# Kernel tuning notes

Measured on AMD Instinct MI355X. Metric: run time of the kernel, lower is better.

The kernel has to match this reference:

```python
import jax, jax.numpy as jnp
import numpy as np

BASE = 10000.0

def rotate_half(x):
    # interleaved pairs: (x0, x1, x2, x3, ...) -> (-x1, x0, -x3, x2, ...)
    x2 = x.reshape(x.shape[:-1] + (-1, 2))
    a, b = x2[..., 0], x2[..., 1]
    return jnp.stack((-b, a), axis=-1).reshape(x.shape)

def rope_tables(seq_len, head_dim, dtype):
    inv_freq = 1.0 / (BASE ** (jnp.arange(0, head_dim, 2, dtype=jnp.float32) / head_dim))
    t = jnp.arange(seq_len, dtype=jnp.float32)
    freqs = jnp.outer(t, inv_freq)                      # [s, head_dim//2]
    cos = jnp.repeat(jnp.cos(freqs), 2, axis=-1)        # '... d -> ... (d 2)'
    sin = jnp.repeat(jnp.sin(freqs), 2, axis=-1)
    # seq_dimension = -3 for [b, s, h, d] tensors -> broadcast over heads
    return cos[:, None, :].astype(dtype), sin[:, None, :].astype(dtype)

def setup_inputs() -> dict:
    key = jax.random.key(0)
    kx, kw1, kw2 = jax.random.split(key, 3)
    b, s, d = 4, 2048, 2048
    h = 16
    x = jax.random.normal(kx, (b, s, d), dtype=jnp.float32)
    # causal mask: True above the diagonal = masked positions
    attn_mask = jnp.triu(jnp.ones((s, s), dtype=bool), k=1)
    Wqkv_w = jax.random.normal(kw1, (d, 3 * d), dtype=jnp.float32) / np.sqrt(d)
    Wqkv_b = jnp.zeros((3 * d,), dtype=jnp.float32)
    Wout_w = jax.random.normal(kw2, (d, d), dtype=jnp.float32) / np.sqrt(d)
    Wout_b = jnp.zeros((d,), dtype=jnp.float32)
    return {"x": x, "attn_mask": attn_mask, "Wqkv_w": Wqkv_w, "Wqkv_b": Wqkv_b,
            "Wout_w": Wout_w, "Wout_b": Wout_b, "num_heads": 16}

def reference(x, attn_mask, Wqkv_w, Wqkv_b, Wout_w, Wout_b, num_heads):
    b, s, d = x.shape
    h = num_heads
    hd = d // h
    qkv = jnp.einsum('bsd,de->bse', x, Wqkv_w) + Wqkv_b        # [b, s, 3d]
    qkv = qkv.reshape(b, s, 3, h, hd)
    q, k, v = qkv[:, :, 0], qkv[:, :, 1], qkv[:, :, 2]          # [b, s, h, hd]
    cos, sin = rope_tables(s, hd, x.dtype)                      # [s, 1, hd]
    q = q * cos + rotate_half(q) * sin
    k = k * cos + rotate_half(k) * sin
    scale = 1.0 / np.sqrt(hd).astype(np.float32)
    scores = jnp.einsum('bqhd,bkhd->bhqk', q, k) * scale        # [b, h, s, s]
    scores = jnp.where(attn_mask, -jnp.inf, scores)
    attn = jax.nn.softmax(scores, axis=-1)
    ctx = jnp.einsum('bhqk,bkhd->bqhd', attn, v)                # [b, s, h, hd]
    ctx = ctx.reshape(b, s, d)
    return jnp.einsum('bsd,de->bse', ctx, Wout_w) + Wout_b
```

## Files before the change

### kernel.cpp

```cpp
#include <hip/hip_runtime.h>

#define BB 4
#define SS 2048
#define DD 2048
#define HH 16
#define HD 128
#define D3 6144

typedef __attribute__((ext_vector_type(8))) short short8;
typedef __attribute__((ext_vector_type(4))) float float4v;

#define MFMA16(a, b, c) __builtin_amdgcn_mfma_f32_16x16x32_bf16(a, b, c, 0, 0, 0)

#define GLL16(g, l)                                                     \
    __builtin_amdgcn_global_load_lds(                                   \
        (__attribute__((address_space(1))) void*)(g),                   \
        (__attribute__((address_space(3))) void*)(l), 16, 0, 0)

__device__ __forceinline__ unsigned short f2b(float f) {
    union { float f; unsigned u; } v;
    v.f = f;
    unsigned r = v.u + 0x7FFFu + ((v.u >> 16) & 1u);
    return (unsigned short)(r >> 16);
}
__device__ __forceinline__ float b2f(unsigned short h) {
    union { unsigned u; float f; } v;
    v.u = ((unsigned)h) << 16;
    return v.f;
}

__global__ void cast_f32_bf16(const float* __restrict__ in,
                              unsigned short* __restrict__ out) {
    int i = (blockIdx.x * 256 + threadIdx.x) * 4;
    float4 v = *(const float4*)(in + i);
    ushort4 o;
    o.x = f2b(v.x); o.y = f2b(v.y); o.z = f2b(v.z); o.w = f2b(v.w);
    *(ushort4*)(out + i) = o;
}

__global__ void transpose_cast(const float* __restrict__ in,
                               unsigned short* __restrict__ out, int R, int C) {
    __shared__ float tile[32][33];
    int c0 = blockIdx.x * 32, r0 = blockIdx.y * 32;
    int tc = threadIdx.x & 31, tr = threadIdx.x >> 5;
#pragma unroll
    for (int i = 0; i < 4; ++i) {
        int r = tr + i * 8;
        tile[r][tc] = in[(size_t)(r0 + r) * C + c0 + tc];
    }
    __syncthreads();
#pragma unroll
    for (int i = 0; i < 4; ++i) {
        int wr = tr + i * 8;
        out[(size_t)(c0 + wr) * R + r0 + tc] = f2b(tile[tc][wr]);
    }
}

__global__ void vtrans(const unsigned short* __restrict__ qkv,
                       unsigned short* __restrict__ vT) {
    __shared__ unsigned short tile[32][33];
    int bh = blockIdx.z, b = bh >> 4, h = bh & 15;
    int s0 = blockIdx.x * 32, d0 = blockIdx.y * 32;
    int tc = threadIdx.x & 31, tr = threadIdx.x >> 5;
    const unsigned short* src = qkv + (size_t)b * SS * D3 + 4096 + h * HD;
#pragma unroll
    for (int i = 0; i < 4; ++i) {
        int sl = tr + i * 8;
        tile[sl][tc] = src[(size_t)(s0 + sl) * D3 + d0 + tc];
    }
    __syncthreads();
    unsigned short* dst = vT + (size_t)bh * HD * SS;
#pragma unroll
    for (int i = 0; i < 4; ++i) {
        int dl = tr + i * 8;
        dst[(size_t)(d0 + dl) * SS + s0 + tc] = tile[tc][dl];
    }
}

template <int BF16OUT>
__global__ __launch_bounds__(512, 2) void gemm256(
    const unsigned short* __restrict__ A,
    const unsigned short* __restrict__ Bt,
    const float* __restrict__ bias,
    void* __restrict__ Cout, int M, int N, int K) {
    __shared__ unsigned short As[2][256 * 64];
    __shared__ unsigned short Bs[2][256 * 64];

    const int nbx = N >> 8;
    const int lin = blockIdx.y * nbx + blockIdx.x;
    const int cpx = (nbx * (M >> 8)) >> 3;
    const int wg = (lin & 7) * cpx + (lin >> 3);
    const int n0 = (wg % nbx) * 256, m0 = (wg / nbx) * 256;

    const int t = threadIdx.x, lane = t & 63, w = t >> 6;
    const int quad = lane >> 4, lr = lane & 15;
    const int wm = (w >> 2) * 128, wn = (w & 3) * 64;

    const int sr = lane >> 3;
    const int ss = (lane & 7) ^ sr;
    const unsigned short* Ag = A + (size_t)(m0 + w * 32 + sr) * K + ss * 8;
    const unsigned short* Bg = Bt + (size_t)(n0 + w * 32 + sr) * K + ss * 8;

    float4v acc[8][4] = {};
    short8 af[4][2], b0[2][2], b1[2][2];

#define STAGE_A(buf, k0)                                                     \
    do {                                                                     \
        _Pragma("unroll") for (int r = 0; r < 4; ++r)                        \
            GLL16(Ag + (k0) + (size_t)r * 8 * K,                             \
                  &As[buf][(w * 32 + r * 8) * 64]);                          \
    } while (0)
#define STAGE_B(buf, k0)                                                     \
    do {                                                                     \
        _Pragma("unroll") for (int r = 0; r < 4; ++r)                        \
            GLL16(Bg + (k0) + (size_t)r * 8 * K,                             \
                  &Bs[buf][(w * 32 + r * 8) * 64]);                          \
    } while (0)
#define LDA(dst, mh)                                                         \
    do {                                                                     \
        _Pragma("unroll") for (int i = 0; i < 4; ++i)                        \
            _Pragma("unroll") for (int kk = 0; kk < 2; ++kk)                 \
                dst[i][kk] = *(const short8*)&As[cur][                       \
                    (wm + (mh)*64 + i * 16 + lr) * 64 +                      \
                    (((kk * 4 + quad) ^ (lr & 7)) * 8)];                     \
    } while (0)
#define LDB(dst, nh)                                                         \
    do {                                                                     \
        _Pragma("unroll") for (int j = 0; j < 2; ++j)                        \
            _Pragma("unroll") for (int kk = 0; kk < 2; ++kk)                 \
                dst[j][kk] = *(const short8*)&Bs[cur][                       \
                    (wn + (nh)*32 + j * 16 + lr) * 64 +                      \
                    (((kk * 4 + quad) ^ (lr & 7)) * 8)];                     \
    } while (0)
#define MM(ar, br, io, jo)                                                   \
    do {                                                                     \
        __builtin_amdgcn_s_setprio(1);                                       \
        _Pragma("unroll") for (int kk = 0; kk < 2; ++kk)                     \
            _Pragma("unroll") for (int i = 0; i < 4; ++i)                    \
                _Pragma("unroll") for (int j = 0; j < 2; ++j)                \
                    acc[(io) + i][(jo) + j] = MFMA16(                        \
                        ar[i][kk], br[j][kk], acc[(io) + i][(jo) + j]);      \
        __builtin_amdgcn_s_setprio(0);                                       \
    } while (0)

    const int NT = K >> 6;
    STAGE_A(0, 0);
    STAGE_B(0, 0);

    for (int tk = 0; tk < NT; ++tk) {
        const int cur = tk & 1, nxt = cur ^ 1;
        const size_t k0n = (size_t)(tk + 1 == NT ? 0 : tk + 1) << 6;

        STAGE_A(nxt, k0n);
        asm volatile("s_waitcnt vmcnt(4)" ::: "memory");
        __builtin_amdgcn_s_barrier();
        __builtin_amdgcn_sched_barrier(0);
        LDA(af, 0);
        LDB(b0, 0);
        __builtin_amdgcn_s_barrier();
        asm volatile("s_waitcnt lgkmcnt(0)" ::: "memory");
        __builtin_amdgcn_sched_barrier(0);
        MM(af, b0, 0, 0);
        __builtin_amdgcn_s_barrier();
        STAGE_B(nxt, k0n);
        LDB(b1, 1);
        __builtin_amdgcn_s_barrier();
        asm volatile("s_waitcnt lgkmcnt(0)" ::: "memory");
        __builtin_amdgcn_sched_barrier(0);
        MM(af, b1, 0, 2);
        __builtin_amdgcn_s_barrier();
        LDA(af, 1);
        __builtin_amdgcn_s_barrier();
        asm volatile("s_waitcnt lgkmcnt(0)" ::: "memory");
        __builtin_amdgcn_sched_barrier(0);
        MM(af, b0, 4, 0);
        __builtin_amdgcn_s_barrier();
        MM(af, b1, 4, 2);
        __builtin_amdgcn_s_barrier();
    }
    asm volatile("s_waitcnt vmcnt(0)" ::: "memory");

#pragma unroll
    for (int jj = 0; jj < 4; ++jj) {
        const int n = n0 + wn + jj * 16 + lr;
        const float bv = bias[n];
#pragma unroll
        for (int ii = 0; ii < 8; ++ii)
#pragma unroll
            for (int r = 0; r < 4; ++r) {
                const int m = m0 + wm + ii * 16 + quad * 4 + r;
                const float v = acc[ii][jj][r] + bv;
                if (BF16OUT)
                    ((unsigned short*)Cout)[(size_t)m * N + n] = f2b(v);
                else
                    ((float*)Cout)[(size_t)m * N + n] = v;
            }
    }
#undef STAGE_A
#undef STAGE_B
#undef LDA
#undef LDB
#undef MM
}

__global__ void rope_kernel(unsigned short* __restrict__ qkv) {
    int tid = blockIdx.x * 256 + threadIdx.x;
    int i4 = tid & 15;
    int h = (tid >> 4) & 15;
    int s = (tid >> 8) & 2047;
    int b = tid >> 19;
    size_t off = ((size_t)(b * SS + s)) * D3 + h * HD + i4 * 8;
    unsigned short* q = qkv + off;
    unsigned short* k = q + 2048;
    short8 qv = *(short8*)q, kv = *(short8*)k;
    const float L2IF = 0.2076205059304601f;
    const float R2PI = 0.15915494309189535f;
    short8 qo, ko;
#pragma unroll
    for (int j = 0; j < 4; ++j) {
        int i = i4 * 4 + j;
        float invr = exp2f(-(float)i * L2IF) * R2PI;
        float rev = (float)s * invr;
        float rr = rev - floorf(rev);
        float sn = __builtin_amdgcn_sinf(rr);
        float cs = __builtin_amdgcn_cosf(rr);
        float a0 = b2f((unsigned short)qv[2 * j]);
        float a1 = b2f((unsigned short)qv[2 * j + 1]);
        qo[2 * j] = (short)f2b(a0 * cs - a1 * sn);
        qo[2 * j + 1] = (short)f2b(a1 * cs + a0 * sn);
        float c0 = b2f((unsigned short)kv[2 * j]);
        float c1 = b2f((unsigned short)kv[2 * j + 1]);
        ko[2 * j] = (short)f2b(c0 * cs - c1 * sn);
        ko[2 * j + 1] = (short)f2b(c1 * cs + c0 * sn);
    }
    *(short8*)q = qo;
    *(short8*)k = ko;
}

__global__ __launch_bounds__(256) void attn_kernel(
    const unsigned short* __restrict__ qkv,
    const unsigned short* __restrict__ vT,
    unsigned short* __restrict__ ctx) {
    __shared__ unsigned short Ks[2][64 * 128];
    __shared__ unsigned short Vs[2][128 * 64];
    __shared__ unsigned short PT[4][32][40];
    const int bh = blockIdx.y, b = bh >> 4, h = bh & 15;
    const int t = threadIdx.x, w = t >> 6, lane = t & 63;
    const int quad = lane >> 4, lr = lane & 15;
    const unsigned short* qbase = qkv + (size_t)b * SS * D3 + h * HD;
    const unsigned short* kbase = qbase + 2048;
    const unsigned short* vtb = vT + (size_t)bh * HD * SS;
    const float SCL2E = 0.12751741769976451f;
    const float NB16 = -23.083120654223414f;
    const int q0a = blockIdx.x * 128;
    const int q0b = (15 - (int)blockIdx.x) * 128;
    const int nta = (q0a >> 6) + 2, ntb = (q0b >> 6) + 2, ntot = nta + ntb;
    const int kr = lane >> 4, kg = lane & 15;
    const int vr = lane >> 3, vg = lane & 7;

    auto stage = [&](int k0, int bi) {
        unsigned short* KD = Ks[bi];
        unsigned short* VD = Vs[bi];
#pragma unroll
        for (int u = 0; u < 4; ++u) {
            int row = w * 16 + u * 4 + kr;
            int g = kg ^ (row & 15);
            GLL16(kbase + (size_t)(k0 + row) * D3 + g * 8,
                  &KD[(w * 16 + u * 4) * 128]);
        }
#pragma unroll
        for (int u = 0; u < 4; ++u) {
            int row = w * 32 + u * 8 + vr;
            int g = vg ^ (row & 7);
            GLL16(vtb + (size_t)row * SS + k0 + g * 8,
                  &VD[(w * 32 + u * 8) * 64]);
        }
    };

    int wq = q0a + w * 32;
    short8 qf[2][4];
#pragma unroll
    for (int m = 0; m < 2; ++m)
#pragma unroll
        for (int c = 0; c < 4; ++c)
            qf[m][c] = *(const short8*)(qbase + (size_t)(wq + m * 16 + lr) * D3 +
                                        c * 32 + quad * 8);

    float4v o[2][8] = {};
    float l_lane[2] = {0.f, 0.f};

    auto epilogue = [&]() {
#pragma unroll
        for (int m = 0; m < 2; ++m) {
            float l = l_lane[m];
            l += __shfl_xor(l, 16);
            l += __shfl_xor(l, 32);
#pragma unroll
            for (int r = 0; r < 4; ++r) {
                float linv = 1.0f / __shfl(l, quad * 4 + r);
#pragma unroll
                for (int dc = 0; dc < 8; ++dc) {
                    float val = o[m][dc][r] * linv;
                    ctx[(size_t)(b * SS + wq + m * 16 + quad * 4 + r) * DD +
                        h * HD + dc * 16 + lr] = f2b(val);
                }
            }
        }
    };

    stage(0, 0);

    for (int it = 0; it < ntot; ++it) {
        __syncthreads();
        int nit = it + 1;
        if (nit < ntot) stage((nit < nta ? nit : nit - nta) * 64, nit & 1);
        int k0 = (it < nta ? it : it - nta) * 64;
        const unsigned short* KB = Ks[it & 1];
        const unsigned short* VB = Vs[it & 1];

        if (k0 <= wq + 31) {
            float4v sc[2][4] = {};
#pragma unroll
            for (int c = 0; c < 4; ++c) {
                short8 kf[4];
#pragma unroll
                for (int ks = 0; ks < 4; ++ks)
                    kf[ks] = *(const short8*)&KB[(ks * 16 + lr) * 128 +
                                                 (((c * 4 + quad) ^ lr) * 8)];
#pragma unroll
                for (int ks = 0; ks < 4; ++ks) {
                    sc[0][ks] = MFMA16(kf[ks], qf[0][c], sc[0][ks]);
                    sc[1][ks] = MFMA16(kf[ks], qf[1][c], sc[1][ks]);
                }
            }
            const bool nm = (k0 + 63 > wq);
#pragma unroll
            for (int kc = 0; kc < 2; ++kc) {
#pragma unroll
                for (int m = 0; m < 2; ++m)
#pragma unroll
                    for (int ks2 = 0; ks2 < 2; ++ks2) {
                        int ks = kc * 2 + ks2;
                        unsigned pk[2];
#pragma unroll
                        for (int rp = 0; rp < 2; ++rp) {
                            unsigned lo = 0, hi = 0;
#pragma unroll
                            for (int rr = 0; rr < 2; ++rr) {
                                int r = rp * 2 + rr;
                                float p = exp2f(fmaf(sc[m][ks][r], SCL2E, NB16));
                                if (nm) {
                                    int key = k0 + ks * 16 + quad * 4 + r;
                                    if (key > wq + m * 16 + lr) p = 0.0f;
                                }
                                l_lane[m] += p;
                                union { float f; unsigned u; } pu;
                                pu.f = p;
                                if (rr == 0) lo = pu.u >> 16;
                                else hi = pu.u >> 16;
                            }
                            pk[rp] = lo | (hi << 16);
                        }
                        uint2 pkk = {pk[0], pk[1]};
                        *(uint2*)&PT[w][m * 16 + lr][ks2 * 16 + quad * 4] = pkk;
                    }
                short8 pf0 = *(const short8*)&PT[w][lr][quad * 8];
                short8 pf1 = *(const short8*)&PT[w][16 + lr][quad * 8];
#pragma unroll
                for (int dc = 0; dc < 8; ++dc) {
                    short8 vf = *(const short8*)&VB[(dc * 16 + lr) * 64 +
                                                    (((kc * 4 + quad) ^ (lr & 7)) * 8)];
                    o[0][dc] = MFMA16(pf0, vf, o[0][dc]);
                    o[1][dc] = MFMA16(pf1, vf, o[1][dc]);
                }
            }
        }

        if (it == nta - 1) {
            epilogue();
#pragma unroll
            for (int m = 0; m < 2; ++m) {
                l_lane[m] = 0.f;
#pragma unroll
                for (int dc = 0; dc < 8; ++dc) o[m][dc] = (float4v){0, 0, 0, 0};
            }
            wq = q0b + w * 32;
#pragma unroll
            for (int m = 0; m < 2; ++m)
#pragma unroll
                for (int c = 0; c < 4; ++c)
                    qf[m][c] = *(const short8*)(qbase +
                                                (size_t)(wq + m * 16 + lr) * D3 +
                                                c * 32 + quad * 8);
        }
    }
    epilogue();
}

extern "C" void kernel_launch(void* const* d_in, const int* in_sizes, int n_in,
                              void* d_out, int out_size, void* d_ws, size_t ws_size,
                              hipStream_t stream) {
    const float* x = (const float*)d_in[0];
    const float* Wqkv_w = (const float*)d_in[2];
    const float* Wqkv_b = (const float*)d_in[3];
    const float* Wout_w = (const float*)d_in[4];
    const float* Wout_b = (const float*)d_in[5];
    float* out = (float*)d_out;

    unsigned short* x_bf = (unsigned short*)d_ws;
    unsigned short* wqkv_t = x_bf + 16777216;
    unsigned short* wout_t = wqkv_t + 12582912;
    unsigned short* qkv = wout_t + 4194304;
    unsigned short* ctx = qkv + 50331648;
    unsigned short* vT = x_bf;

    cast_f32_bf16<<<16384, 256, 0, stream>>>(x, x_bf);
    transpose_cast<<<dim3(192, 64), 256, 0, stream>>>(Wqkv_w, wqkv_t, 2048, 6144);
    transpose_cast<<<dim3(64, 64), 256, 0, stream>>>(Wout_w, wout_t, 2048, 2048);
    gemm256<1><<<dim3(24, 32), 512, 0, stream>>>(x_bf, wqkv_t, Wqkv_b, qkv,
                                                 8192, 6144, 2048);
    rope_kernel<<<8192, 256, 0, stream>>>(qkv);
    vtrans<<<dim3(64, 4, 64), 256, 0, stream>>>(qkv, vT);
    attn_kernel<<<dim3(8, 64), 256, 0, stream>>>(qkv, vT, ctx);
    gemm256<0><<<dim3(8, 32), 512, 0, stream>>>(ctx, wout_t, Wout_b, out,
                                                8192, 2048, 2048);
}
```

Baseline: 786.0 us.

## Restructure GEMM into four-stage K=32 pipeline with prefetch three tiles ahead

The 256x256 GEMM's K tile shrinks from 64 to 32 and the shared-memory ring grows from two buffers to four. Global-to-LDS loads now run three iterations ahead, gated by vmcnt(8). The LDS swizzle is reworked for the narrower 32-element rows, and the XCD-aware block remapping is replaced by a plain blockIdx mapping. This aims to hide global-load latency better at the same LDS footprint, but it doubles the number of loop iterations and barriers and drops the L2-locality block ordering.

```diff
diff --git a/kernel.cpp b/kernel.cpp
--- a/kernel.cpp
+++ b/kernel.cpp
@@ -83,99 +83,90 @@
     const unsigned short* __restrict__ Bt,
     const float* __restrict__ bias,
     void* __restrict__ Cout, int M, int N, int K) {
-    __shared__ unsigned short As[2][256 * 64];
-    __shared__ unsigned short Bs[2][256 * 64];
-
-    const int nbx = N >> 8;
-    const int lin = blockIdx.y * nbx + blockIdx.x;
-    const int cpx = (nbx * (M >> 8)) >> 3;
-    const int wg = (lin & 7) * cpx + (lin >> 3);
-    const int n0 = (wg % nbx) * 256, m0 = (wg / nbx) * 256;
-
+    __shared__ unsigned short As[4][256 * 32];
+    __shared__ unsigned short Bs[4][256 * 32];
+
+    const int n0 = blockIdx.x * 256, m0 = blockIdx.y * 256;
     const int t = threadIdx.x, lane = t & 63, w = t >> 6;
     const int quad = lane >> 4, lr = lane & 15;
     const int wm = (w >> 2) * 128, wn = (w & 3) * 64;
 
-    const int sr = lane >> 3;
-    const int ss = (lane & 7) ^ sr;
-    const unsigned short* Ag = A + (size_t)(m0 + w * 32 + sr) * K + ss * 8;
-    const unsigned short* Bg = Bt + (size_t)(n0 + w * 32 + sr) * K + ss * 8;
+    const int sr = lane >> 2;
+    const int sc = ((lane & 3) ^ ((lane >> 3) & 3)) * 8;
+    const unsigned short* Ag = A + (size_t)(m0 + w * 16 + sr) * K + sc;
+    const unsigned short* Bg = Bt + (size_t)(n0 + w * 16 + sr) * K + sc;
+
+    const int rsw = (quad ^ ((lr >> 1) & 3)) * 8;
 
     float4v acc[8][4] = {};
-    short8 af[4][2], b0[2][2], b1[2][2];
-
-#define STAGE_A(buf, k0)                                                     \
-    do {                                                                     \
-        _Pragma("unroll") for (int r = 0; r < 4; ++r)                        \
-            GLL16(Ag + (k0) + (size_t)r * 8 * K,                             \
-                  &As[buf][(w * 32 + r * 8) * 64]);                          \
-    } while (0)
-#define STAGE_B(buf, k0)                                                     \
-    do {                                                                     \
-        _Pragma("unroll") for (int r = 0; r < 4; ++r)                        \
-            GLL16(Bg + (k0) + (size_t)r * 8 * K,                             \
-                  &Bs[buf][(w * 32 + r * 8) * 64]);                          \
-    } while (0)
+    short8 af0[4], af1[4], b0[2], b1[2];
+
+#define SA(buf, rb, k0) \
+    GLL16(Ag + (size_t)(rb) * K + (k0), &As[buf][((rb) + w * 16) * 32])
+#define SB(buf, rb, k0) \
+    GLL16(Bg + (size_t)(rb) * K + (k0), &Bs[buf][((rb) + w * 16) * 32])
+#define STAGE_A(buf, k0) do { SA(buf, 0, k0); SA(buf, 128, k0); } while (0)
+#define STAGE_B(buf, k0) do { SB(buf, 0, k0); SB(buf, 128, k0); } while (0)
 #define LDA(dst, mh)                                                         \
     do {                                                                     \
         _Pragma("unroll") for (int i = 0; i < 4; ++i)                        \
-            _Pragma("unroll") for (int kk = 0; kk < 2; ++kk)                 \
-                dst[i][kk] = *(const short8*)&As[cur][                       \
-                    (wm + (mh)*64 + i * 16 + lr) * 64 +                      \
-                    (((kk * 4 + quad) ^ (lr & 7)) * 8)];                     \
+            dst[i] = *(const short8*)&As[cur][                               \
+                (wm + (mh)*64 + i * 16 + lr) * 32 + rsw];                    \
     } while (0)
 #define LDB(dst, nh)                                                         \
     do {                                                                     \
         _Pragma("unroll") for (int j = 0; j < 2; ++j)                        \
-            _Pragma("unroll") for (int kk = 0; kk < 2; ++kk)                 \
-                dst[j][kk] = *(const short8*)&Bs[cur][                       \
-                    (wn + (nh)*32 + j * 16 + lr) * 64 +                      \
-                    (((kk * 4 + quad) ^ (lr & 7)) * 8)];                     \
+            dst[j] = *(const short8*)&Bs[cur][                               \
+                (wn + (nh)*32 + j * 16 + lr) * 32 + rsw];                    \
     } while (0)
 #define MM(ar, br, io, jo)                                                   \
     do {                                                                     \
         __builtin_amdgcn_s_setprio(1);                                       \
-        _Pragma("unroll") for (int kk = 0; kk < 2; ++kk)                     \
-            _Pragma("unroll") for (int i = 0; i < 4; ++i)                    \
-                _Pragma("unroll") for (int j = 0; j < 2; ++j)                \
-                    acc[(io) + i][(jo) + j] = MFMA16(                        \
-                        ar[i][kk], br[j][kk], acc[(io) + i][(jo) + j]);      \
+        _Pragma("unroll") for (int i = 0; i < 4; ++i)                        \
+            _Pragma("unroll") for (int j = 0; j < 2; ++j)                    \
+                acc[(io) + i][(jo) + j] = MFMA16(                            \
+                    ar[i], br[j], acc[(io) + i][(jo) + j]);                  \
         __builtin_amdgcn_s_setprio(0);                                       \
     } while (0)
-
-    const int NT = K >> 6;
-    STAGE_A(0, 0);
-    STAGE_B(0, 0);
+#define WAIT_LGKM0()                                                         \
+    do {                                                                     \
+        asm volatile("s_waitcnt lgkmcnt(0)" ::: "memory");                   \
+        __builtin_amdgcn_sched_barrier(0);                                   \
+    } while (0)
+
+    const int NT = K >> 5;
+    STAGE_A(0, 0);  STAGE_B(0, 0);
+    STAGE_A(1, 32); STAGE_B(1, 32);
+    STAGE_A(2, 64); STAGE_B(2, 64);
+    asm volatile("s_waitcnt vmcnt(8)" ::: "memory");
+    __builtin_amdgcn_s_barrier();
 
     for (int tk = 0; tk < NT; ++tk) {
-        const int cur = tk & 1, nxt = cur ^ 1;
-        const size_t k0n = (size_t)(tk + 1 == NT ? 0 : tk + 1) << 6;
-
-        STAGE_A(nxt, k0n);
-        asm volatile("s_waitcnt vmcnt(4)" ::: "memory");
-        __builtin_amdgcn_s_barrier();
-        __builtin_amdgcn_sched_barrier(0);
-        LDA(af, 0);
+        const int cur = tk & 3;
+        const int b3 = (tk + 3) & 3;
+        int t3 = tk + 3; if (t3 >= NT) t3 -= NT;
+        const int k3 = t3 << 5;
+
+        LDA(af0, 0);
         LDB(b0, 0);
-        __builtin_amdgcn_s_barrier();
-        asm volatile("s_waitcnt lgkmcnt(0)" ::: "memory");
-        __builtin_amdgcn_sched_barrier(0);
-        MM(af, b0, 0, 0);
-        __builtin_amdgcn_s_barrier();
-        STAGE_B(nxt, k0n);
+        STAGE_A(b3, k3);
+        __builtin_amdgcn_s_barrier();
+        WAIT_LGKM0();
+        MM(af0, b0, 0, 0);
+        __builtin_amdgcn_s_barrier();
         LDB(b1, 1);
-        __builtin_amdgcn_s_barrier();
-        asm volatile("s_waitcnt lgkmcnt(0)" ::: "memory");
-        __builtin_amdgcn_sched_barrier(0);
-        MM(af, b1, 0, 2);
-        __builtin_amdgcn_s_barrier();
-        LDA(af, 1);
-        __builtin_amdgcn_s_barrier();
-        asm volatile("s_waitcnt lgkmcnt(0)" ::: "memory");
-        __builtin_amdgcn_sched_barrier(0);
-        MM(af, b0, 4, 0);
-        __builtin_amdgcn_s_barrier();
-        MM(af, b1, 4, 2);
+        STAGE_B(b3, k3);
+        __builtin_amdgcn_s_barrier();
+        WAIT_LGKM0();
+        MM(af0, b1, 0, 2);
+        __builtin_amdgcn_s_barrier();
+        LDA(af1, 1);
+        __builtin_amdgcn_s_barrier();
+        WAIT_LGKM0();
+        MM(af1, b1, 4, 2);
+        __builtin_amdgcn_s_barrier();
+        MM(af1, b0, 4, 0);
+        asm volatile("s_waitcnt vmcnt(8)" ::: "memory");
         __builtin_amdgcn_s_barrier();
     }
     asm volatile("s_waitcnt vmcnt(0)" ::: "memory");
@@ -196,11 +187,14 @@
                     ((float*)Cout)[(size_t)m * N + n] = v;
             }
     }
+#undef SA
+#undef SB
 #undef STAGE_A
 #undef STAGE_B
 #undef LDA
 #undef LDB
 #undef MM
+#undef WAIT_LGKM0
 }
 
 __global__ void rope_kernel(unsigned short* __restrict__ qkv) {
```

Result: faster. 737.3 us (-6.2%).
